# Performance work log

Hardware: AMD Instinct MI355X
Metric: run time of the kernel (lower is better)

Reference implementation:

```python
import jax, jax.numpy as jnp
import numpy as np

DIM = 768
HEADS = 8
HIDDEN = 3072
B, Hs, Ws = 16, 32, 32
N = Hs * Ws
LN_EPS = 1e-5


def setup_inputs() -> dict:
    key = jax.random.key(0)
    ks = jax.random.split(key, 10)
    s = lambda *sh: 0.02
    return {
        "x": jax.random.normal(ks[0], (B, N, DIM), jnp.float32),
        "Wq": jax.random.normal(ks[1], (DIM, DIM), jnp.float32) * 0.02,
        "temperature": jnp.ones((HEADS, 1, 1), jnp.float32),
        "fc1_w": jax.random.normal(ks[2], (HIDDEN, DIM), jnp.float32) * 0.02,
        "fc1_b": jnp.zeros((HIDDEN,), jnp.float32),
        "dw_w": jax.random.normal(ks[3], (HIDDEN, 1, 3, 3), jnp.float32) * 0.1,
        "dw_b": jnp.zeros((HIDDEN,), jnp.float32),
        "gamma": jnp.ones((HIDDEN,), jnp.float32),
        "fc2_w": jax.random.normal(ks[4], (DIM, HIDDEN), jnp.float32) * 0.02,
        "fc2_b": jnp.zeros((DIM,), jnp.float32),
        "ln_w": jnp.ones((DIM,), jnp.float32),
        "ln_b": jnp.zeros((DIM,), jnp.float32),
        "H": Hs,
        "W": Ws,
    }


def _dwconv(x, w, b, H, W):
    # x: (B, N, hidden) -> depthwise 3x3, pad 1 -> (B, N, hidden)
    Bn, Nn, Ch = x.shape
    img = x.transpose(0, 2, 1).reshape(Bn, Ch, H, W)
    out = jax.lax.conv_general_dilated(
        img, w, window_strides=(1, 1), padding=((1, 1), (1, 1)),
        dimension_numbers=("NCHW", "OIHW", "NCHW"), feature_group_count=Ch)
    out = out + b[None, :, None, None]
    return out.reshape(Bn, Ch, Nn).transpose(0, 2, 1)


def _layernorm(x, w, b):
    mu = x.mean(-1, keepdims=True)
    var = ((x - mu) ** 2).mean(-1, keepdims=True)
    return (x - mu) * jax.lax.rsqrt(var + LN_EPS) * w + b


def reference(x, Wq, temperature, fc1_w, fc1_b, dw_w, dw_b, gamma,
              fc2_w, fc2_b, ln_w, ln_b, H, W):
    # gpd_ratio == active_ratio == 1 -> pre/post scalings cancel
    Bn, Nn, C = x.shape
    h = temperature.shape[0]
    Ch = C // h
    # q/k/v heads: (B, h, N, Ch)
    q = (x @ Wq.T).reshape(Bn, Nn, h, Ch).transpose(0, 2, 1, 3)
    kv = x.reshape(Bn, Nn, h, Ch).transpose(0, 2, 1, 3)
    # channel attention: softmax over N, pool k over Ch, sigmoid gate
    qs = jax.nn.softmax(q, axis=-2).transpose(0, 1, 3, 2)      # (B,h,Ch,N)
    kp = jax.nn.softmax(kv, axis=-2).mean(-1, keepdims=True)    # (B,h,N,1)
    attn = jax.nn.sigmoid(qs @ kp) * temperature                # (B,h,Ch,1)
    # MLP on v (== x after scaling cancels): fc1 -> dwconv residual -> fc2 -> LN
    h1 = x @ fc1_w.T + fc1_b                                    # (B,N,hidden)
    h2 = gamma * _dwconv(h1, dw_w, dw_b, H, W) + h1
    v = _layernorm(h2 @ fc2_w.T + fc2_b, ln_w, ln_b)            # (B,N,C)
    v = v.reshape(Bn, Nn, h, Ch).transpose(0, 2, 1, 3)          # (B,h,N,Ch)
    prod = attn * v.transpose(0, 1, 3, 2)                       # (B,h,Ch,N)
    out = prod.transpose(0, 3, 1, 2).reshape(Bn, Nn, C)
    return out, prod.transpose(0, 1, 3, 2)
```

## Files before the change

kernel.cpp:

```cpp
#include <hip/hip_runtime.h>

#define BATCH 16
#define SEQ   1024
#define DIM   768
#define NHEAD 8
#define CHD   96
#define HID   3072
#define MTOT  (BATCH * SEQ)

using u16 = unsigned short;
typedef __attribute__((ext_vector_type(8))) short bf16x8;
typedef __attribute__((ext_vector_type(4))) float f32x4;

#define AS1 __attribute__((address_space(1)))
#define AS3 __attribute__((address_space(3)))

__device__ inline float bf2f(u16 u) {
    union { unsigned int i; float f; } v; v.i = ((unsigned int)u) << 16; return v.f;
}
__device__ inline u16 f2bf(float f) {
    union { float f; unsigned int i; } v; v.f = f;
    unsigned int r = v.i + 0x7FFFu + ((v.i >> 16) & 1u);
    return (u16)(r >> 16);
}

__device__ inline void gld16(const void* g, void* l) {
    __builtin_amdgcn_global_load_lds((AS1 const void*)g, (AS3 void*)l, 16, 0, 0);
}

__device__ inline void storeC(float* p, float v) { *p = v; }
__device__ inline void storeC(u16* p, float v) { *p = f2bf(v); }

template <bool HAS_BIAS, typename TC>
__global__ __launch_bounds__(256) void gemm_mfma(const u16* __restrict__ A,
                                                 const u16* __restrict__ B,
                                                 const float* __restrict__ bias,
                                                 TC* __restrict__ C,
                                                 int M, int N, int K) {
    __shared__ u16 As[128 * 32];
    __shared__ u16 Bs[128 * 32];
    const int tid = threadIdx.x;
    const int lane = tid & 63;
    const int m0 = blockIdx.y << 7, n0 = blockIdx.x << 7;
    const int wave = tid >> 6;
    const int wm = (wave >> 1) << 6, wn = (wave & 1) << 6;

    f32x4 acc[4][4] = {};

    const int row0 = tid >> 2;
    const int kc8 = (tid & 3) << 3;
    const u16* pa0 = A + (size_t)(m0 + row0) * K + kc8;
    const u16* pa1 = A + (size_t)(m0 + 64 + row0) * K + kc8;
    const u16* pb0 = B + (size_t)(n0 + row0) * K + kc8;
    const u16* pb1 = B + (size_t)(n0 + 64 + row0) * K + kc8;
    u16* da0 = &As[tid * 8];
    u16* da1 = &As[(256 + tid) * 8];
    u16* db0 = &Bs[tid * 8];
    u16* db1 = &Bs[(256 + tid) * 8];

    const int lrow = lane & 15;
    const int kgrp = (lane >> 4) << 3;

    for (int k0 = 0; k0 < K; k0 += 32) {
        gld16(pa0 + k0, da0);
        gld16(pa1 + k0, da1);
        gld16(pb0 + k0, db0);
        gld16(pb1 + k0, db1);
        __syncthreads();

        bf16x8 af[4], bfr[4];
#pragma unroll
        for (int i = 0; i < 4; ++i)
            af[i] = *(const bf16x8*)&As[(wm + i * 16 + lrow) * 32 + kgrp];
#pragma unroll
        for (int j = 0; j < 4; ++j)
            bfr[j] = *(const bf16x8*)&Bs[(wn + j * 16 + lrow) * 32 + kgrp];
#pragma unroll
        for (int i = 0; i < 4; ++i)
#pragma unroll
            for (int j = 0; j < 4; ++j)
                acc[i][j] = __builtin_amdgcn_mfma_f32_16x16x32_bf16(af[i], bfr[j], acc[i][j], 0, 0, 0);
        __syncthreads();
    }

    const int crow = (lane >> 4) << 2;
    const int ccol = lane & 15;
#pragma unroll
    for (int i = 0; i < 4; ++i) {
        const int gm = m0 + wm + i * 16 + crow;
#pragma unroll
        for (int j = 0; j < 4; ++j) {
            const int gn = n0 + wn + j * 16 + ccol;
            const float bv = HAS_BIAS ? bias[gn] : 0.f;
#pragma unroll
            for (int r = 0; r < 4; ++r)
                storeC(C + (size_t)(gm + r) * N + gn, acc[i][j][r] + bv);
        }
    }
}

__global__ __launch_bounds__(256) void cvt_f2bf(const float* __restrict__ in,
                                                u16* __restrict__ out, int n4) {
    int i = blockIdx.x * 256 + threadIdx.x;
    if (i >= n4) return;
    float4 v = reinterpret_cast<const float4*>(in)[i];
    ushort4 o;
    o.x = f2bf(v.x); o.y = f2bf(v.y); o.z = f2bf(v.z); o.w = f2bf(v.w);
    reinterpret_cast<ushort4*>(out)[i] = o;
}

template <typename T>
__global__ __launch_bounds__(256) void colsm_stats(const T* __restrict__ X,
                                                   float* __restrict__ Mo,
                                                   float* __restrict__ So,
                                                   int ncols) {
    const int tid = threadIdx.x, lane = tid & 63, chunk = tid >> 6;
    const int b = blockIdx.y;
    const int j = blockIdx.x * 64 + lane;
    const T* p = X + (size_t)b * SEQ * ncols + j;
    float m = -3.0e38f, s = 0.f;
    const int nEnd = (chunk + 1) << 8;
    for (int n = chunk << 8; n < nEnd; ++n) {
        float raw;
        if constexpr (sizeof(T) == 2) raw = bf2f(p[(size_t)n * ncols]);
        else raw = p[(size_t)n * ncols];
        float nm = fmaxf(m, raw);
        s = s * __expf(m - nm) + __expf(raw - nm);
        m = nm;
    }
    __shared__ float ms[4][64], ss[4][64];
    ms[chunk][lane] = m; ss[chunk][lane] = s;
    __syncthreads();
    if (tid < 64) {
        float M = fmaxf(fmaxf(ms[0][lane], ms[1][lane]), fmaxf(ms[2][lane], ms[3][lane]));
        float S = ss[0][lane] * __expf(ms[0][lane] - M) + ss[1][lane] * __expf(ms[1][lane] - M) +
                  ss[2][lane] * __expf(ms[2][lane] - M) + ss[3][lane] * __expf(ms[3][lane] - M);
        Mo[b * ncols + j] = M;
        So[b * ncols + j] = S;
    }
}

__global__ __launch_bounds__(256) void kp_k(const float* __restrict__ x,
                                            const float* __restrict__ Mx,
                                            const float* __restrict__ Sx,
                                            float* __restrict__ kp) {
    const int n = blockIdx.x, b = blockIdx.y, tid = threadIdx.x;
    __shared__ float p[DIM];
    const float* row = x + ((size_t)b * SEQ + n) * DIM;
#pragma unroll
    for (int q = 0; q < 3; ++q) {
        int j = tid + (q << 8);
        p[j] = __expf(row[j] - Mx[b * DIM + j]) / Sx[b * DIM + j];
    }
    __syncthreads();
    if (tid < NHEAD) {
        float s = 0.f;
        for (int c = 0; c < CHD; ++c) s += p[tid * CHD + c];
        kp[((size_t)b * NHEAD + tid) * SEQ + n] = s * (1.f / (float)CHD);
    }
}

__global__ __launch_bounds__(256) void attn_k(const u16* __restrict__ Q,
                                              const float* __restrict__ Mq,
                                              const float* __restrict__ Sq,
                                              const float* __restrict__ kp,
                                              const float* __restrict__ temp,
                                              float* __restrict__ attnv) {
    const int tid = threadIdx.x, lane = tid & 63, chunk = tid >> 6;
    const int b = blockIdx.y;
    const int j = blockIdx.x * 64 + lane;
    const int h = j / CHD;
    const float mq = Mq[b * DIM + j];
    const u16* qp = Q + (size_t)b * SEQ * DIM + j;
    const float* kpp = kp + ((size_t)b * NHEAD + h) * SEQ;
    float acc = 0.f;
    const int nEnd = (chunk + 1) << 8;
    for (int n = chunk << 8; n < nEnd; ++n)
        acc += __expf(bf2f(qp[(size_t)n * DIM]) - mq) * kpp[n];
    __shared__ float accs[4][64];
    accs[chunk][lane] = acc;
    __syncthreads();
    if (tid < 64) {
        float a = accs[0][lane] + accs[1][lane] + accs[2][lane] + accs[3][lane];
        float z = a / Sq[b * DIM + j];
        attnv[b * DIM + j] = temp[h] / (1.f + __expf(-z));
    }
}

__global__ __launch_bounds__(128) void dwconv_v(const u16* __restrict__ h1,
                                                const float* __restrict__ w,
                                                const float* __restrict__ dwb,
                                                const float* __restrict__ gamma,
                                                u16* __restrict__ h2) {
    const int g = blockIdx.x * 128 + threadIdx.x;
    const int y = blockIdx.y >> 2;
    const int xw0 = (blockIdx.y & 3) << 3;
    const int b = blockIdx.z;
    const int ch0 = g << 3;

    float wreg[8][9], bias2[8];
#pragma unroll
    for (int c = 0; c < 8; ++c) {
        const float gm = gamma[ch0 + c];
#pragma unroll
        for (int k = 0; k < 9; ++k) wreg[c][k] = gm * w[(ch0 + c) * 9 + k];
        wreg[c][4] += 1.0f;
        bias2[c] = gm * dwb[ch0 + c];
    }

    float acc[8][8];
#pragma unroll
    for (int xo = 0; xo < 8; ++xo)
#pragma unroll
        for (int c = 0; c < 8; ++c) acc[xo][c] = bias2[c];

    const u16* base = h1 + (size_t)b * SEQ * HID + ch0;
#pragma unroll
    for (int dy = 0; dy < 3; ++dy) {
        const int yy = y + dy - 1;
        if ((unsigned)yy > 31u) continue;
#pragma unroll
        for (int cr = -1; cr <= 8; ++cr) {
            const int col = xw0 + cr;
            if ((unsigned)col > 31u) continue;
            const uint4 v = *reinterpret_cast<const uint4*>(
                base + (size_t)((yy << 5) + col) * HID);
            float f[8];
            f[0] = bf2f((u16)(v.x & 0xffff)); f[1] = bf2f((u16)(v.x >> 16));
            f[2] = bf2f((u16)(v.y & 0xffff)); f[3] = bf2f((u16)(v.y >> 16));
            f[4] = bf2f((u16)(v.z & 0xffff)); f[5] = bf2f((u16)(v.w & 0xffff) * 0 + (u16)(v.z >> 16));
            f[6] = bf2f((u16)(v.w & 0xffff)); f[7] = bf2f((u16)(v.w >> 16));
            const int xlo = cr > 0 ? cr - 1 : 0;
            const int xhi = cr < 7 ? cr + 1 : 7;
#pragma unroll
            for (int xo = 0; xo < 8; ++xo) {
                if (xo < xlo || xo > xhi) continue;
                const int dx = cr - xo + 1;
#pragma unroll
                for (int c = 0; c < 8; ++c)
                    acc[xo][c] += f[c] * wreg[c][dy * 3 + dx];
            }
        }
    }

#pragma unroll
    for (int xo = 0; xo < 8; ++xo) {
        const int n = (y << 5) + xw0 + xo;
        uint4 o;
        o.x = (unsigned)f2bf(acc[xo][0]) | ((unsigned)f2bf(acc[xo][1]) << 16);
        o.y = (unsigned)f2bf(acc[xo][2]) | ((unsigned)f2bf(acc[xo][3]) << 16);
        o.z = (unsigned)f2bf(acc[xo][4]) | ((unsigned)f2bf(acc[xo][5]) << 16);
        o.w = (unsigned)f2bf(acc[xo][6]) | ((unsigned)f2bf(acc[xo][7]) << 16);
        *reinterpret_cast<uint4*>(h2 + ((size_t)b * SEQ + n) * HID + ch0) = o;
    }
}

__global__ __launch_bounds__(256) void ln_out_k(const u16* __restrict__ vpre,
                                                const float* __restrict__ lnw,
                                                const float* __restrict__ lnb,
                                                const float* __restrict__ attnv,
                                                float* __restrict__ out,
                                                float* __restrict__ out2) {
    const int n = blockIdx.x, b = blockIdx.y, tid = threadIdx.x;
    __shared__ float red[4];
    const u16* row = vpre + ((size_t)b * SEQ + n) * DIM;
    float v[3];
    float s = 0.f;
#pragma unroll
    for (int q = 0; q < 3; ++q) { v[q] = bf2f(row[tid + (q << 8)]); s += v[q]; }
#pragma unroll
    for (int o = 32; o; o >>= 1) s += __shfl_down(s, o, 64);
    if ((tid & 63) == 0) red[tid >> 6] = s;
    __syncthreads();
    const float mu = (red[0] + red[1] + red[2] + red[3]) * (1.f / (float)DIM);
    __syncthreads();
    float vs = 0.f;
#pragma unroll
    for (int q = 0; q < 3; ++q) { float d = v[q] - mu; vs += d * d; }
#pragma unroll
    for (int o = 32; o; o >>= 1) vs += __shfl_down(vs, o, 64);
    if ((tid & 63) == 0) red[tid >> 6] = vs;
    __syncthreads();
    const float rstd = rsqrtf((red[0] + red[1] + red[2] + red[3]) * (1.f / (float)DIM) + 1e-5f);
    const float* at = attnv + b * DIM;
    float* orow = out + ((size_t)b * SEQ + n) * DIM;
#pragma unroll
    for (int q = 0; q < 3; ++q) {
        int j = tid + (q << 8);
        float o = (v[q] - mu) * rstd * lnw[j] + lnb[j];
        o *= at[j];
        orow[j] = o;
        int h = j / CHD, c = j - h * CHD;
        out2[(((size_t)b * NHEAD + h) * SEQ + n) * CHD + c] = o;
    }
}

extern "C" void kernel_launch(void* const* d_in, const int* in_sizes, int n_in,
                              void* d_out, int out_size, void* d_ws, size_t ws_size,
                              hipStream_t stream) {
    const float* x     = (const float*)d_in[0];
    const float* Wq    = (const float*)d_in[1];
    const float* temp  = (const float*)d_in[2];
    const float* fc1w  = (const float*)d_in[3];
    const float* fc1b  = (const float*)d_in[4];
    const float* dww   = (const float*)d_in[5];
    const float* dwb   = (const float*)d_in[6];
    const float* gamma = (const float*)d_in[7];
    const float* fc2w  = (const float*)d_in[8];
    const float* fc2b  = (const float*)d_in[9];
    const float* lnw   = (const float*)d_in[10];
    const float* lnb   = (const float*)d_in[11];

    float* out  = (float*)d_out;
    float* out2 = out + (size_t)BATCH * SEQ * DIM;

    char* ws = (char*)d_ws;
    u16* xb     = (u16*)ws;
    u16* h1     = (u16*)(ws + 25165824);
    u16* Wqb    = (u16*)(ws + 125829120);
    u16* fc1wb  = (u16*)(ws + 127008768);
    u16* fc2wb  = (u16*)(ws + 131727360);
    float* Mx   = (float*)(ws + 136445952);
    float* Sx   = Mx + BATCH * DIM;
    float* Mq   = Sx + BATCH * DIM;
    float* Sq   = Mq + BATCH * DIM;
    float* kp   = Sq + BATCH * DIM;
    float* attnv = kp + BATCH * NHEAD * SEQ;
    u16* vpreb  = xb;

    u16* Qb = (u16*)d_out;
    u16* h2 = (u16*)d_out;

    cvt_f2bf<<<(MTOT * DIM / 4 + 255) / 256, 256, 0, stream>>>(x, xb, MTOT * DIM / 4);
    cvt_f2bf<<<(DIM * DIM / 4 + 255) / 256, 256, 0, stream>>>(Wq, Wqb, DIM * DIM / 4);
    cvt_f2bf<<<(HID * DIM / 4 + 255) / 256, 256, 0, stream>>>(fc1w, fc1wb, HID * DIM / 4);
    cvt_f2bf<<<(DIM * HID / 4 + 255) / 256, 256, 0, stream>>>(fc2w, fc2wb, DIM * HID / 4);

    gemm_mfma<false, u16><<<dim3(DIM / 128, MTOT / 128), 256, 0, stream>>>(
        xb, Wqb, nullptr, Qb, MTOT, DIM, DIM);
    colsm_stats<float><<<dim3(DIM / 64, BATCH), 256, 0, stream>>>(x, Mx, Sx, DIM);
    colsm_stats<u16><<<dim3(DIM / 64, BATCH), 256, 0, stream>>>(Qb, Mq, Sq, DIM);
    kp_k<<<dim3(SEQ, BATCH), 256, 0, stream>>>(x, Mx, Sx, kp);
    attn_k<<<dim3(DIM / 64, BATCH), 256, 0, stream>>>(Qb, Mq, Sq, kp, temp, attnv);

    gemm_mfma<true, u16><<<dim3(HID / 128, MTOT / 128), 256, 0, stream>>>(
        xb, fc1wb, fc1b, h1, MTOT, HID, DIM);
    dwconv_v<<<dim3(3, 128, BATCH), 128, 0, stream>>>(h1, dww, dwb, gamma, h2);
    gemm_mfma<true, u16><<<dim3(DIM / 128, MTOT / 128), 256, 0, stream>>>(
        h2, fc2wb, fc2b, vpreb, MTOT, DIM, HID);
    ln_out_k<<<dim3(SEQ, BATCH), 256, 0, stream>>>(vpreb, lnw, lnb, attnv, out, out2);
}
```

Before: 464.4 us.

## Replace GEMM with 256x256 tile, 4-stage LDS pipeline, swizzle and XCD remap

Swaps the 128x128 single-buffered MFMA GEMM for a 256x256-tile kernel with 512 threads. Global-to-LDS loads are issued three tiles ahead through a 4-slot ring, gated by explicit vmcnt waits. LDS columns are XOR-swizzled to avoid bank conflicts, and workgroup ids are remapped across XCDs for cache locality. This targets load latency and synchronization stalls in the three big GEMMs, at the cost of 128KB LDS per block and heavy register use, which limits occupancy. It also cleans up an odd expression in the dwconv bf16 unpack.

```diff
diff --git a/kernel.cpp b/kernel.cpp
--- a/kernel.cpp
+++ b/kernel.cpp
@@ -28,65 +28,101 @@
     __builtin_amdgcn_global_load_lds((AS1 const void*)g, (AS3 void*)l, 16, 0, 0);
 }
 
-__device__ inline void storeC(float* p, float v) { *p = v; }
-__device__ inline void storeC(u16* p, float v) { *p = f2bf(v); }
-
-template <bool HAS_BIAS, typename TC>
-__global__ __launch_bounds__(256) void gemm_mfma(const u16* __restrict__ A,
-                                                 const u16* __restrict__ B,
-                                                 const float* __restrict__ bias,
-                                                 TC* __restrict__ C,
-                                                 int M, int N, int K) {
-    __shared__ u16 As[128 * 32];
-    __shared__ u16 Bs[128 * 32];
+template <bool HAS_BIAS>
+__global__ __launch_bounds__(512, 2) void gemm256(const u16* __restrict__ A,
+                                                  const u16* __restrict__ B,
+                                                  const float* __restrict__ bias,
+                                                  u16* __restrict__ C,
+                                                  int M, int N, int K) {
+    __shared__ u16 lds[4][2][256 * 32];
     const int tid = threadIdx.x;
     const int lane = tid & 63;
-    const int m0 = blockIdx.y << 7, n0 = blockIdx.x << 7;
-    const int wave = tid >> 6;
-    const int wm = (wave >> 1) << 6, wn = (wave & 1) << 6;
-
-    f32x4 acc[4][4] = {};
-
-    const int row0 = tid >> 2;
-    const int kc8 = (tid & 3) << 3;
-    const u16* pa0 = A + (size_t)(m0 + row0) * K + kc8;
-    const u16* pa1 = A + (size_t)(m0 + 64 + row0) * K + kc8;
-    const u16* pb0 = B + (size_t)(n0 + row0) * K + kc8;
-    const u16* pb1 = B + (size_t)(n0 + 64 + row0) * K + kc8;
-    u16* da0 = &As[tid * 8];
-    u16* da1 = &As[(256 + tid) * 8];
-    u16* db0 = &Bs[tid * 8];
-    u16* db1 = &Bs[(256 + tid) * 8];
+    const int wid = tid >> 6;
+    const int wm = (wid >> 2) << 7;
+    const int wn = (wid & 3) << 6;
+
+    const int nwg = gridDim.x;
+    const int wg = blockIdx.x;
+    const int lid = (wg & 7) * (nwg >> 3) + (wg >> 3);
+    const int nbx = N >> 8;
+    const int mb = lid / nbx, nb = lid - mb * nbx;
+    const int m0 = mb << 8, n0 = nb << 8;
+
+    const int srow = tid >> 2;
+    const int scol = (((tid & 3) << 4) ^ ((srow & 3) << 4)) >> 1;
+    const u16* pa0 = A + (size_t)(m0 + srow) * K + scol;
+    const u16* pa1 = A + (size_t)(m0 + 128 + srow) * K + scol;
+    const u16* pb0 = B + (size_t)(n0 + srow) * K + scol;
+    const u16* pb1 = B + (size_t)(n0 + 128 + srow) * K + scol;
 
     const int lrow = lane & 15;
-    const int kgrp = (lane >> 4) << 3;
-
-    for (int k0 = 0; k0 < K; k0 += 32) {
-        gld16(pa0 + k0, da0);
-        gld16(pa1 + k0, da1);
-        gld16(pb0 + k0, db0);
-        gld16(pb1 + k0, db1);
-        __syncthreads();
-
-        bf16x8 af[4], bfr[4];
+    const int swcol = ((((lane >> 4) << 4) ^ ((lrow & 3) << 4)) >> 1);
+
+    f32x4 acc[8][4] = {};
+
+#define STAGE256(bf, kk) do {                                   \
+    gld16(pa0 + (kk), &lds[bf][0][tid * 8]);                    \
+    gld16(pa1 + (kk), &lds[bf][0][(512 + tid) * 8]);            \
+    gld16(pb0 + (kk), &lds[bf][1][tid * 8]);                    \
+    gld16(pb1 + (kk), &lds[bf][1][(512 + tid) * 8]);            \
+} while (0)
+
+    const int NT = K >> 5;
+    STAGE256(0, 0);
+    STAGE256(1, 32);
+    STAGE256(2, 64);
+
+    for (int T = 0; T < NT; ++T) {
+        const int rem = NT - 1 - T;
+        if (rem >= 2)      asm volatile("s_waitcnt vmcnt(8)" ::: "memory");
+        else if (rem == 1) asm volatile("s_waitcnt vmcnt(4)" ::: "memory");
+        else               asm volatile("s_waitcnt vmcnt(0)" ::: "memory");
+        __builtin_amdgcn_sched_barrier(0);
+        __builtin_amdgcn_s_barrier();
+        __builtin_amdgcn_sched_barrier(0);
+
+        const u16* Ab = lds[T & 3][0];
+        const u16* Bb = lds[T & 3][1];
+
+        bf16x8 bfr[4], afr[4];
+#pragma unroll
+        for (int j = 0; j < 4; ++j)
+            bfr[j] = *(const bf16x8*)&Bb[(wn + j * 16 + lrow) * 32 + swcol];
 #pragma unroll
         for (int i = 0; i < 4; ++i)
-            af[i] = *(const bf16x8*)&As[(wm + i * 16 + lrow) * 32 + kgrp];
-#pragma unroll
-        for (int j = 0; j < 4; ++j)
-            bfr[j] = *(const bf16x8*)&Bs[(wn + j * 16 + lrow) * 32 + kgrp];
+            afr[i] = *(const bf16x8*)&Ab[(wm + i * 16 + lrow) * 32 + swcol];
+
+        if (T + 3 < NT) STAGE256((T + 3) & 3, (T + 3) * 32);
+
+        asm volatile("s_waitcnt lgkmcnt(0)" ::: "memory");
+        __builtin_amdgcn_sched_barrier(0);
+        __builtin_amdgcn_s_setprio(1);
 #pragma unroll
         for (int i = 0; i < 4; ++i)
 #pragma unroll
             for (int j = 0; j < 4; ++j)
-                acc[i][j] = __builtin_amdgcn_mfma_f32_16x16x32_bf16(af[i], bfr[j], acc[i][j], 0, 0, 0);
-        __syncthreads();
-    }
-
-    const int crow = (lane >> 4) << 2;
-    const int ccol = lane & 15;
-#pragma unroll
-    for (int i = 0; i < 4; ++i) {
+                acc[i][j] = __builtin_amdgcn_mfma_f32_16x16x32_bf16(afr[i], bfr[j], acc[i][j], 0, 0, 0);
+        __builtin_amdgcn_s_setprio(0);
+
+        bf16x8 afr2[4];
+#pragma unroll
+        for (int i = 0; i < 4; ++i)
+            afr2[i] = *(const bf16x8*)&Ab[(wm + (i + 4) * 16 + lrow) * 32 + swcol];
+        asm volatile("s_waitcnt lgkmcnt(0)" ::: "memory");
+        __builtin_amdgcn_sched_barrier(0);
+        __builtin_amdgcn_s_setprio(1);
+#pragma unroll
+        for (int i = 0; i < 4; ++i)
+#pragma unroll
+            for (int j = 0; j < 4; ++j)
+                acc[i + 4][j] = __builtin_amdgcn_mfma_f32_16x16x32_bf16(afr2[i], bfr[j], acc[i + 4][j], 0, 0, 0);
+        __builtin_amdgcn_s_setprio(0);
+    }
+#undef STAGE256
+
+    const int crow = (lane >> 4) << 2, ccol = lane & 15;
+#pragma unroll
+    for (int i = 0; i < 8; ++i) {
         const int gm = m0 + wm + i * 16 + crow;
 #pragma unroll
         for (int j = 0; j < 4; ++j) {
@@ -94,7 +130,7 @@
             const float bv = HAS_BIAS ? bias[gn] : 0.f;
 #pragma unroll
             for (int r = 0; r < 4; ++r)
-                storeC(C + (size_t)(gm + r) * N + gn, acc[i][j][r] + bv);
+                C[(size_t)(gm + r) * N + gn] = f2bf(acc[i][j][r] + bv);
         }
     }
 }
@@ -228,7 +264,7 @@
             float f[8];
             f[0] = bf2f((u16)(v.x & 0xffff)); f[1] = bf2f((u16)(v.x >> 16));
             f[2] = bf2f((u16)(v.y & 0xffff)); f[3] = bf2f((u16)(v.y >> 16));
-            f[4] = bf2f((u16)(v.z & 0xffff)); f[5] = bf2f((u16)(v.w & 0xffff) * 0 + (u16)(v.z >> 16));
+            f[4] = bf2f((u16)(v.z & 0xffff)); f[5] = bf2f((u16)(v.z >> 16));
             f[6] = bf2f((u16)(v.w & 0xffff)); f[7] = bf2f((u16)(v.w >> 16));
             const int xlo = cr > 0 ? cr - 1 : 0;
             const int xhi = cr < 7 ? cr + 1 : 7;
@@ -336,17 +372,17 @@
     cvt_f2bf<<<(HID * DIM / 4 + 255) / 256, 256, 0, stream>>>(fc1w, fc1wb, HID * DIM / 4);
     cvt_f2bf<<<(DIM * HID / 4 + 255) / 256, 256, 0, stream>>>(fc2w, fc2wb, DIM * HID / 4);
 
-    gemm_mfma<false, u16><<<dim3(DIM / 128, MTOT / 128), 256, 0, stream>>>(
+    gemm256<false><<<(MTOT / 256) * (DIM / 256), 512, 0, stream>>>(
         xb, Wqb, nullptr, Qb, MTOT, DIM, DIM);
     colsm_stats<float><<<dim3(DIM / 64, BATCH), 256, 0, stream>>>(x, Mx, Sx, DIM);
     colsm_stats<u16><<<dim3(DIM / 64, BATCH), 256, 0, stream>>>(Qb, Mq, Sq, DIM);
     kp_k<<<dim3(SEQ, BATCH), 256, 0, stream>>>(x, Mx, Sx, kp);
     attn_k<<<dim3(DIM / 64, BATCH), 256, 0, stream>>>(Qb, Mq, Sq, kp, temp, attnv);
 
-    gemm_mfma<true, u16><<<dim3(HID / 128, MTOT / 128), 256, 0, stream>>>(
+    gemm256<true><<<(MTOT / 256) * (HID / 256), 512, 0, stream>>>(
         xb, fc1wb, fc1b, h1, MTOT, HID, DIM);
     dwconv_v<<<dim3(3, 128, BATCH), 128, 0, stream>>>(h1, dww, dwb, gamma, h2);
-    gemm_mfma<true, u16><<<dim3(DIM / 128, MTOT / 128), 256, 0, stream>>>(
+    gemm256<true><<<(MTOT / 256) * (DIM / 256), 512, 0, stream>>>(
         h2, fc2wb, fc2b, vpreb, MTOT, DIM, HID);
     ln_out_k<<<dim3(SEQ, BATCH), 256, 0, stream>>>(vpreb, lnw, lnb, attnv, out, out2);
 }
```

Result: faster. 411.4 us (-11.4%).
